# Kernel tuning notes

Measured on AMD Instinct MI355X. Metric: run time of the kernel, lower is better.

Reference implementation:

```python
import jax, jax.numpy as jnp
import numpy as np

N_VERTS = 1_000_000
N_EDGES = 3_000_000
H, W = 1024, 1024
MAX_DEPTH = 10.0
DEPTH_SCALE = 1.0
CREGU = 2000.0


def setup_inputs() -> dict:
    key = jax.random.key(0)
    k1, k2, k3, k4, k5, k6 = jax.random.split(key, 6)
    # mesh vertices roughly in a unit-radius blob
    vertices = jax.random.normal(k1, (N_VERTS, 3), dtype=jnp.float32) * 0.5
    vertices_ref = vertices + 0.01 * jax.random.normal(k2, (N_VERTS, 3), dtype=jnp.float32)
    quaternion = jax.random.normal(k3, (4,), dtype=jnp.float32) + jnp.array([0., 0., 0., 1.], jnp.float32)
    translation = jax.random.normal(k4, (3,), dtype=jnp.float32) * 0.05
    hand_image = jax.random.uniform(k5, (H, W), dtype=jnp.float32) * MAX_DEPTH
    # camera per MeshDepthFitterEnergy.setImage: R = diag(1,-1,-1), focal = 2*W
    object_center = np.zeros(3, np.float32)
    object_radius = 0.5
    camera_center = object_center + np.array([-0.5, 0.0, 5.0], np.float32) * object_radius
    R = np.array([[1., 0., 0.], [0., -1., 0.], [0., 0., -1.]], np.float32)
    T = -R.T.dot(camera_center)
    focal = 2.0 * W
    intrinsic = jnp.array([[focal, 0., W / 2.], [0., focal, H / 2.], [0., 0., 1.]], jnp.float32)
    extrinsic = jnp.array(np.column_stack((R, T)), jnp.float32)
    edges = jax.random.randint(k6, (N_EDGES, 2), 0, N_VERTS, dtype=jnp.int64)
    return {"vertices": vertices, "vertices_ref": vertices_ref, "quaternion": quaternion,
            "translation": translation, "hand_image": hand_image,
            "intrinsic": intrinsic, "extrinsic": extrinsic, "edges": edges}


def _qrot(q, v):
    # q: [4] (x,y,z,w) normalized; v: [N,3]
    qvec = q[:3]
    uv = jnp.cross(jnp.broadcast_to(qvec, v.shape), v)
    uuv = jnp.cross(jnp.broadcast_to(qvec, v.shape), uv)
    return v + 2.0 * (q[3] * uv + uuv)


def _forward(vertices, vertices_ref, quaternion, translation, hand_image,
             intrinsic, extrinsic, edges):
    # rigid transform
    q = quaternion / jnp.linalg.norm(quaternion)
    v_centered = vertices - jnp.mean(vertices, axis=0, keepdims=True)
    v_t = _qrot(q, v_centered) + translation  # [N,3]
    # camera projection: P_cam = R x + T ; pix = K P_cam / z
    p_cam = v_t @ extrinsic[:, :3].T + extrinsic[:, 3]  # [N,3]
    proj = p_cam @ intrinsic.T
    z = p_cam[:, 2] * DEPTH_SCALE
    u = proj[:, 0] / proj[:, 2]
    v = proj[:, 1] / proj[:, 2]
    xi = jnp.clip(jnp.round(u), 0, W - 1).astype(jnp.int32)
    yi = jnp.clip(jnp.round(v), 0, H - 1).astype(jnp.int32)
    flat = yi * W + xi  # [N]
    # z-buffer: scatter-min of per-vertex depth (invalid/behind-camera -> MAX_DEPTH)
    zvalid = jnp.where(z > 0, z, MAX_DEPTH)
    depth_flat = jnp.full((H * W,), MAX_DEPTH, dtype=vertices.dtype).at[flat].min(zvalid)
    depth = jnp.clip(depth_flat, 0.0, MAX_DEPTH).reshape(H, W)
    diff_image = (depth - hand_image) ** 2
    e_data = jnp.sum(diff_image)
    # Laplacian rigid energy: cregu * || L (V - Vref) ||^2 over the edge graph
    dv = vertices - vertices_ref
    src, dst = edges[:, 0], edges[:, 1]
    deg = jax.ops.segment_sum(jnp.ones((N_EDGES,), vertices.dtype), src, num_segments=N_VERTS)
    neigh = jax.ops.segment_sum(dv[dst], src, num_segments=N_VERTS)  # [N,3]
    ldv = deg[:, None] * dv - neigh
    e_rigid = CREGU * jnp.sum(ldv ** 2)
    return e_data + e_rigid


def reference(vertices, vertices_ref, quaternion, translation, hand_image,
              intrinsic, extrinsic, edges):
    return _forward(vertices, vertices_ref, quaternion, translation, hand_image,
                    intrinsic, extrinsic, edges)
```

## Files before the change

kernel.cpp:

```cpp
#include <hip/hip_runtime.h>

#define W_IMG 1024
#define H_IMG 1024
#define HW_IMG (W_IMG * H_IMG)
#define NV 1000000
#define NE 3000000
#define NV4 (NE / 2)
#define MAX_DEPTH 10.0f
#define CREGU 2000.0f

#define NBUCKET 245
#define BSHIFT 12
#define BSIZE 4096

#define PREP_BLOCKS 2048
#define HIST_BLOCKS 250
#define HIST_V4 6000
#define SCAT_V4 2048
#define SCAT_EDGES (SCAT_V4 * 2)
#define SCAT_BLOCKS ((NV4 + SCAT_V4 - 1) / SCAT_V4)
#define GEO_BLOCKS 1024
#define TSIZE 2048
#define EDATA_BLOCKS 256

#define QXY 4096.0f
#define IQXY 2.44140625e-4f
#define QZ 2048.0f
#define IQZ 4.8828125e-4f
#define BXY2 1024
#define BZ2 512

typedef int v4i __attribute__((ext_vector_type(4)));

__device__ __forceinline__ unsigned pack_dv32(float x, float y, float z) {
    x = fminf(fmaxf(x, -0.2f), 0.2f);
    y = fminf(fmaxf(y, -0.2f), 0.2f);
    z = fminf(fmaxf(z, -0.2f), 0.2f);
    unsigned px = (unsigned)((int)rintf(x * QXY) + BXY2);
    unsigned py = (unsigned)((int)rintf(y * QXY) + BXY2);
    unsigned pz = (unsigned)((int)rintf(z * QZ) + BZ2);
    return (px << 21) | (py << 10) | pz;
}

__device__ __forceinline__ unsigned long long expand_dv(unsigned p) {
    unsigned long long x = (p >> 21) & 0x7FFu;
    unsigned long long y = (p >> 10) & 0x7FFu;
    unsigned long long z = p & 0x3FFu;
    return (x << 44) | (y << 24) | (z << 6) | 1ull;
}

__device__ __forceinline__ float block_sum_256(float v, float* smem) {
#pragma unroll
    for (int o = 32; o > 0; o >>= 1) v += __shfl_down(v, o, 64);
    int lane = threadIdx.x & 63;
    int wid  = threadIdx.x >> 6;
    if (lane == 0) smem[wid] = v;
    __syncthreads();
    float r = 0.f;
    if (threadIdx.x == 0) r = smem[0] + smem[1] + smem[2] + smem[3];
    __syncthreads();
    return r;
}

__device__ __forceinline__ void prefix245(const unsigned* __restrict__ src,
                                          unsigned* dst) {
    int t = threadIdx.x;
    unsigned h = (t < NBUCKET) ? src[t] : 0u;
    dst[t] = h;
    __syncthreads();
#pragma unroll
    for (int o = 1; o < 256; o <<= 1) {
        unsigned v = (t >= o) ? dst[t - o] : 0u;
        __syncthreads();
        dst[t] += v;
        __syncthreads();
    }
    unsigned excl = dst[t] - h;
    __syncthreads();
    dst[t] = excl;
    __syncthreads();
}

__global__ void k_prep(const float* __restrict__ verts,
                       const float* __restrict__ verts_ref,
                       unsigned* __restrict__ pdv32,
                       unsigned* __restrict__ depth_bits, int ncd,
                       unsigned long long* __restrict__ neigh, int modeA,
                       const v4i* __restrict__ edges2,
                       unsigned* __restrict__ hist,
                       float4* __restrict__ partial) {
    __shared__ float smem[4];
    __shared__ unsigned lh[NBUCKET];
    int i = blockIdx.x * blockDim.x + threadIdx.x;
    int stride = gridDim.x * blockDim.x;

    float sx = 0.f, sy = 0.f, sz = 0.f;
    for (int j = i; j < NV; j += stride) {
        float x = verts[3 * j + 0];
        float y = verts[3 * j + 1];
        float z = verts[3 * j + 2];
        sx += x; sy += y; sz += z;
        pdv32[j] = pack_dv32(x - verts_ref[3 * j + 0],
                             y - verts_ref[3 * j + 1],
                             z - verts_ref[3 * j + 2]);
        if (!modeA) neigh[j] = 0ull;
    }
    size_t totd = (size_t)ncd * HW_IMG;
    for (size_t j = i; j < totd; j += stride) depth_bits[j] = 0x41200000u;

    if (modeA && blockIdx.x < HIST_BLOCKS) {
        for (int t = threadIdx.x; t < NBUCKET; t += blockDim.x) lh[t] = 0u;
        __syncthreads();
        int base = blockIdx.x * HIST_V4;
        for (int k = threadIdx.x; k < HIST_V4; k += blockDim.x) {
            v4i e = __builtin_nontemporal_load(&edges2[base + k]);
            atomicAdd(&lh[(unsigned)e.x >> BSHIFT], 1u);
            atomicAdd(&lh[(unsigned)e.z >> BSHIFT], 1u);
        }
        __syncthreads();
        for (int t = threadIdx.x; t < NBUCKET; t += blockDim.x)
            if (lh[t]) atomicAdd(&hist[t], lh[t]);
    }

    float bx = block_sum_256(sx, smem);
    float by = block_sum_256(sy, smem);
    float bz = block_sum_256(sz, smem);
    if (threadIdx.x == 0) {
        float4 p; p.x = bx; p.y = by; p.z = bz; p.w = 0.f;
        partial[blockIdx.x] = p;
    }
}

union SMem {
    struct {
        unsigned h_key[TSIZE];
        unsigned h_val[TSIZE];
        float rsm[8];
    } geo;
    struct {
        unsigned long long sort[SCAT_EDGES];
        unsigned sLh[NBUCKET];
        unsigned sPfx[256];
        unsigned sDelta[NBUCKET];
        unsigned sOff[256];
    } sc;
};

__global__ void k_main(const v4i* __restrict__ edges2,
                       const unsigned* __restrict__ pdv32,
                       unsigned long long* __restrict__ rec,
                       const unsigned* __restrict__ hist,
                       unsigned* __restrict__ reserve,
                       unsigned long long* __restrict__ neigh, int modeA,
                       const float* __restrict__ verts,
                       const float* __restrict__ quat,
                       const float* __restrict__ trans,
                       const float* __restrict__ intr,
                       const float* __restrict__ extr,
                       const float4* __restrict__ partial,
                       unsigned* __restrict__ depth_bits, int ncd) {
    __shared__ SMem sm;

    if (blockIdx.x >= GEO_BLOCKS) {
        int sb = blockIdx.x - GEO_BLOCKS;
        int base = sb * SCAT_V4;
        if (modeA) {
            for (int t = threadIdx.x; t < NBUCKET; t += blockDim.x) sm.sc.sLh[t] = 0u;
            __syncthreads();

            v4i e[8];
            unsigned r0[8], r1[8];
#pragma unroll
            for (int k = 0; k < 8; ++k) {
                int idx = base + k * 256 + (int)threadIdx.x;
                if (idx < NV4) {
                    e[k] = __builtin_nontemporal_load(&edges2[idx]);
                    r0[k] = atomicAdd(&sm.sc.sLh[(unsigned)e[k].x >> BSHIFT], 1u);
                    r1[k] = atomicAdd(&sm.sc.sLh[(unsigned)e[k].z >> BSHIFT], 1u);
                }
            }
            __syncthreads();
            prefix245(sm.sc.sLh, sm.sc.sPfx);
            prefix245(hist, sm.sc.sOff);
            for (int t = threadIdx.x; t < NBUCKET; t += blockDim.x) {
                unsigned c = sm.sc.sLh[t];
                unsigned res = c ? atomicAdd(&reserve[t], c) : 0u;
                sm.sc.sDelta[t] = sm.sc.sOff[t] + res - sm.sc.sPfx[t];
            }
            __syncthreads();
#pragma unroll
            for (int k = 0; k < 8; ++k) {
                int idx = base + k * 256 + (int)threadIdx.x;
                if (idx < NV4) {
                    unsigned s0 = (unsigned)e[k].x;
                    unsigned b0 = s0 >> BSHIFT;
                    unsigned long long rec0 =
                        ((unsigned long long)b0 << 56) |
                        ((unsigned long long)pdv32[e[k].y] << 12) |
                        (s0 & (BSIZE - 1));
                    sm.sc.sort[sm.sc.sPfx[b0] + r0[k]] = rec0;
                    unsigned s1 = (unsigned)e[k].z;
                    unsigned b1 = s1 >> BSHIFT;
                    unsigned long long rec1 =
                        ((unsigned long long)b1 << 56) |
                        ((unsigned long long)pdv32[e[k].w] << 12) |
                        (s1 & (BSIZE - 1));
                    sm.sc.sort[sm.sc.sPfx[b1] + r1[k]] = rec1;
                }
            }
            __syncthreads();
            int nrec = (base + SCAT_V4 <= NV4) ? SCAT_EDGES
                                               : 2 * (NV4 - base);
#pragma unroll
            for (int k = 0; k < 16; ++k) {
                int t = k * 256 + (int)threadIdx.x;
                if (t < nrec) {
                    unsigned long long r = sm.sc.sort[t];
                    unsigned bin = (unsigned)(r >> 56);
                    rec[(size_t)t + sm.sc.sDelta[bin]] = r;
                }
            }
        } else {
#pragma unroll
            for (int k = 0; k < 8; ++k) {
                int idx = base + k * 256 + (int)threadIdx.x;
                if (idx < NV4) {
                    v4i e = __builtin_nontemporal_load(&edges2[idx]);
                    atomicAdd(&neigh[(size_t)(unsigned)e.x], expand_dv(pdv32[e.y]));
                    atomicAdd(&neigh[(size_t)(unsigned)e.z], expand_dv(pdv32[e.w]));
                }
            }
        }
        return;
    }

    int gb = blockIdx.x;
    for (int s = threadIdx.x; s < TSIZE; s += blockDim.x) {
        sm.geo.h_key[s] = 0xFFFFFFFFu;
        sm.geo.h_val[s] = 0xFFFFFFFFu;
    }
    __syncthreads();

    float sx = 0.f, sy = 0.f, sz = 0.f;
    for (int p = threadIdx.x; p < PREP_BLOCKS; p += blockDim.x) {
        float4 v = partial[p];
        sx += v.x; sy += v.y; sz += v.z;
    }
    float bx = block_sum_256(sx, sm.geo.rsm);
    float by = block_sum_256(sy, sm.geo.rsm);
    float bz = block_sum_256(sz, sm.geo.rsm);
    if (threadIdx.x == 0) {
        const float inv_nv = 1.0f / (float)NV;
        sm.geo.rsm[4] = bx * inv_nv;
        sm.geo.rsm[5] = by * inv_nv;
        sm.geo.rsm[6] = bz * inv_nv;
    }
    __syncthreads();
    float mx = sm.geo.rsm[4], my = sm.geo.rsm[5], mz = sm.geo.rsm[6];

    float qx = quat[0], qy = quat[1], qz = quat[2], qw = quat[3];
    float qn = rsqrtf(qx * qx + qy * qy + qz * qz + qw * qw);
    qx *= qn; qy *= qn; qz *= qn; qw *= qn;
    float t0 = trans[0], t1 = trans[1], t2 = trans[2];
    float e0 = extr[0], e1 = extr[1], e2 = extr[2],  e3 = extr[3];
    float e4 = extr[4], e5 = extr[5], e6 = extr[6],  e7 = extr[7];
    float e8 = extr[8], e9 = extr[9], e10 = extr[10], e11 = extr[11];
    float i0 = intr[0], i1 = intr[1], i2 = intr[2];
    float i3 = intr[3], i4 = intr[4], i5 = intr[5];
    float i6 = intr[6], i7 = intr[7], i8 = intr[8];

    unsigned* __restrict__ db = depth_bits + (size_t)(gb & (ncd - 1)) * HW_IMG;

    int stride = GEO_BLOCKS * blockDim.x;
    for (int j = gb * blockDim.x + threadIdx.x; j < NV; j += stride) {
        float vx = __builtin_nontemporal_load(&verts[3 * j + 0]) - mx;
        float vy = __builtin_nontemporal_load(&verts[3 * j + 1]) - my;
        float vz = __builtin_nontemporal_load(&verts[3 * j + 2]) - mz;

        float uvx = qy * vz - qz * vy;
        float uvy = qz * vx - qx * vz;
        float uvz = qx * vy - qy * vx;
        float uuvx = qy * uvz - qz * uvy;
        float uuvy = qz * uvx - qx * uvz;
        float uuvz = qx * uvy - qy * uvx;
        float tx = vx + 2.f * (qw * uvx + uuvx) + t0;
        float ty = vy + 2.f * (qw * uvy + uuvy) + t1;
        float tz = vz + 2.f * (qw * uvz + uuvz) + t2;

        float px = e0 * tx + e1 * ty + e2  * tz + e3;
        float py = e4 * tx + e5 * ty + e6  * tz + e7;
        float pz = e8 * tx + e9 * ty + e10 * tz + e11;

        float pr0 = i0 * px + i1 * py + i2 * pz;
        float pr1 = i3 * px + i4 * py + i5 * pz;
        float pr2 = i6 * px + i7 * py + i8 * pz;

        float u = pr0 / pr2;
        float v = pr1 / pr2;
        float ru = rintf(u);
        float rv = rintf(v);
        bool border = (ru < 0.f) | (ru > (float)(W_IMG - 1)) |
                      (rv < 0.f) | (rv > (float)(H_IMG - 1));
        float xf = fminf(fmaxf(ru, 0.f), (float)(W_IMG - 1));
        float yf = fminf(fmaxf(rv, 0.f), (float)(H_IMG - 1));
        unsigned flat = (unsigned)((int)yf * W_IMG + (int)xf);

        if (pz > 0.f) {
            unsigned zbits = __float_as_uint(pz);
            bool direct = !border;
            if (border) {
                unsigned slot = (flat * 2654435761u) >> 21;
                bool done = false;
#pragma unroll
                for (int p = 0; p < 4; ++p) {
                    unsigned old = atomicCAS(&sm.geo.h_key[slot], 0xFFFFFFFFu, flat);
                    if (old == 0xFFFFFFFFu || old == flat) {
                        atomicMin(&sm.geo.h_val[slot], zbits);
                        done = true;
                        break;
                    }
                    slot = (slot + 1) & (TSIZE - 1);
                }
                direct = !done;
            }
            if (direct) atomicMin(&db[flat], zbits);
        }
    }
    __syncthreads();
    for (int s = threadIdx.x; s < TSIZE; s += blockDim.x) {
        unsigned k = sm.geo.h_key[s];
        if (k != 0xFFFFFFFFu) atomicMin(&db[k], sm.geo.h_val[s]);
    }
}

__global__ void k_energy(const unsigned* __restrict__ depth_bits, int ncd,
                         const float* __restrict__ hand,
                         const unsigned* __restrict__ pdv32,
                         const unsigned long long* __restrict__ rec,
                         const unsigned* __restrict__ hist,
                         const unsigned long long* __restrict__ neigh, int modeA,
                         float* out) {
    __shared__ unsigned long long acc[BSIZE];
    __shared__ unsigned sOff[256];
    __shared__ float smem[4];

    if (blockIdx.x < NBUCKET) {
        int b = blockIdx.x;
        int vbase = b * BSIZE;
        int nvert = (NV - vbase < BSIZE) ? (NV - vbase) : BSIZE;
        if (modeA) {
            prefix245(hist, sOff);
            unsigned start = sOff[b];
            unsigned count = hist[b];
            for (int v = threadIdx.x; v < BSIZE; v += blockDim.x) acc[v] = 0ull;
            __syncthreads();
            for (unsigned i = threadIdx.x; i < count; i += blockDim.x) {
                unsigned long long r = rec[start + i];
                unsigned p = (unsigned)(r >> 12);
                unsigned s = (unsigned)(r & (BSIZE - 1));
                atomicAdd(&acc[s], expand_dv(p));
            }
            __syncthreads();
        }
        float lacc = 0.f;
        for (int v = threadIdx.x; v < nvert; v += blockDim.x) {
            unsigned long long n = modeA ? acc[v] : neigh[(size_t)vbase + v];
            int cnt = (int)(n & 63ull);
            int rz  = (int)((n >> 6)  & 0x3FFFFull);
            int ry  = (int)((n >> 24) & 0xFFFFFull);
            int rx  = (int)(n >> 44);
            float nx = (float)(rx - cnt * BXY2) * IQXY;
            float ny = (float)(ry - cnt * BXY2) * IQXY;
            float nz = (float)(rz - cnt * BZ2)  * IQZ;
            unsigned p = pdv32[vbase + v];
            float dx = (float)((int)((p >> 21) & 0x7FFu) - BXY2) * IQXY;
            float dy = (float)((int)((p >> 10) & 0x7FFu) - BXY2) * IQXY;
            float dz = (float)((int)(p & 0x3FFu) - BZ2) * IQZ;
            float dg = (float)cnt;
            float lx = dg * dx - nx;
            float ly = dg * dy - ny;
            float lz = dg * dz - nz;
            lacc += lx * lx + ly * ly + lz * lz;
        }
        float bsum = block_sum_256(lacc, smem);
        if (threadIdx.x == 0) atomicAdd(out, CREGU * bsum);
    } else {
        int eb = blockIdx.x - NBUCKET;
        int i = eb * blockDim.x + threadIdx.x;
        int stride = EDATA_BLOCKS * blockDim.x;
        float accd = 0.f;
        for (int j = i; j < HW_IMG; j += stride) {
            float dmin = __uint_as_float(depth_bits[j]);
            for (int c = 1; c < ncd; ++c)
                dmin = fminf(dmin, __uint_as_float(depth_bits[(size_t)c * HW_IMG + j]));
            float depth = fminf(fmaxf(dmin, 0.f), MAX_DEPTH);
            float diff = depth - hand[j];
            accd += diff * diff;
        }
        float bsum = block_sum_256(accd, smem);
        if (threadIdx.x == 0) atomicAdd(out, bsum);
    }
}

extern "C" void kernel_launch(void* const* d_in, const int* in_sizes, int n_in,
                              void* d_out, int out_size, void* d_ws, size_t ws_size,
                              hipStream_t stream) {
    const float* verts     = (const float*)d_in[0];
    const float* verts_ref = (const float*)d_in[1];
    const float* quat      = (const float*)d_in[2];
    const float* trans     = (const float*)d_in[3];
    const float* hand      = (const float*)d_in[4];
    const float* intr      = (const float*)d_in[5];
    const float* extr      = (const float*)d_in[6];
    const int*   edges     = (const int*)d_in[7];
    float* out = (float*)d_out;

    char* ws = (char*)d_ws;
    const size_t OFF_BINS = (size_t)NV * 4;
    const size_t OFF_PART = OFF_BINS + 4096;
    const size_t OFF_REC  = OFF_PART + (size_t)PREP_BLOCKS * 16;

    const size_t A_FIX = OFF_REC + (size_t)NE * 8;
    const size_t B_FIX = OFF_REC + (size_t)NV * 8;

    int modeA, ncd;
    size_t OFF_DEPTH;
    if (ws_size >= A_FIX + 4ull * HW_IMG * 4)      { modeA = 1; ncd = 4; OFF_DEPTH = A_FIX; }
    else if (ws_size >= A_FIX + 2ull * HW_IMG * 4) { modeA = 1; ncd = 2; OFF_DEPTH = A_FIX; }
    else if (ws_size >= A_FIX + 1ull * HW_IMG * 4) { modeA = 1; ncd = 1; OFF_DEPTH = A_FIX; }
    else if (ws_size >= B_FIX + 4ull * HW_IMG * 4) { modeA = 0; ncd = 4; OFF_DEPTH = B_FIX; }
    else if (ws_size >= B_FIX + 2ull * HW_IMG * 4) { modeA = 0; ncd = 2; OFF_DEPTH = B_FIX; }
    else                                           { modeA = 0; ncd = 1; OFF_DEPTH = B_FIX; }

    unsigned*           pdv32      = (unsigned*)ws;
    unsigned*           hist       = (unsigned*)(ws + OFF_BINS);
    unsigned*           reserve    = hist + 256;
    float4*             partial    = (float4*)(ws + OFF_PART);
    unsigned long long* rec        = (unsigned long long*)(ws + OFF_REC);
    unsigned long long* neigh      = (unsigned long long*)(ws + OFF_REC);
    unsigned*           depth_bits = (unsigned*)(ws + OFF_DEPTH);

    const int B = 256;

    hipMemsetAsync(ws + OFF_BINS, 0, 4096, stream);
    hipMemsetAsync(d_out, 0, sizeof(float), stream);

    k_prep<<<PREP_BLOCKS, B, 0, stream>>>(verts, verts_ref, pdv32, depth_bits,
                                          ncd, neigh, modeA, (const v4i*)edges,
                                          hist, partial);
    k_main<<<GEO_BLOCKS + SCAT_BLOCKS, B, 0, stream>>>(
        (const v4i*)edges, pdv32, rec, hist, reserve, neigh, modeA,
        verts, quat, trans, intr, extr, partial, depth_bits, ncd);
    k_energy<<<NBUCKET + EDATA_BLOCKS, B, 0, stream>>>(
        depth_bits, ncd, hand, pdv32, rec, hist, neigh, modeA, out);
}
```

Baseline: 234.4 us.

## Drop memsets and global histogram atomics, vectorize prep and depth loops

Zeroing of the output and the reserve counters moves into k_prep, which removes the two hipMemsetAsync calls. The global atomic histogram becomes per-block partial histograms; each scatter block reduces these partials and takes a prefix, and block 0 publishes the bucket offsets for k_energy. Vertex prep, depth-buffer init and the data-energy loop now use float4/uint4 accesses, and the atomic-neighbour fallback mode is removed. The trade-off is that every scatter block redundantly reads 250 histogram partials, and the old smaller-workspace fallback path is gone.

```diff
diff --git a/kernel.cpp b/kernel.cpp
--- a/kernel.cpp
+++ b/kernel.cpp
@@ -4,6 +4,7 @@
 #define H_IMG 1024
 #define HW_IMG (W_IMG * H_IMG)
 #define NV 1000000
+#define NQUAD (NV / 4)
 #define NE 3000000
 #define NV4 (NE / 2)
 #define MAX_DEPTH 10.0f
@@ -13,7 +14,7 @@
 #define BSHIFT 12
 #define BSIZE 4096
 
-#define PREP_BLOCKS 2048
+#define PREP_BLOCKS 1024
 #define HIST_BLOCKS 250
 #define HIST_V4 6000
 #define SCAT_V4 2048
@@ -62,54 +63,65 @@
     return r;
 }
 
-__device__ __forceinline__ void prefix245(const unsigned* __restrict__ src,
-                                          unsigned* dst) {
+__device__ __forceinline__ void prefix_excl_256(unsigned h, unsigned* buf) {
     int t = threadIdx.x;
-    unsigned h = (t < NBUCKET) ? src[t] : 0u;
-    dst[t] = h;
+    buf[t] = h;
     __syncthreads();
 #pragma unroll
     for (int o = 1; o < 256; o <<= 1) {
-        unsigned v = (t >= o) ? dst[t - o] : 0u;
-        __syncthreads();
-        dst[t] += v;
-        __syncthreads();
-    }
-    unsigned excl = dst[t] - h;
-    __syncthreads();
-    dst[t] = excl;
-    __syncthreads();
-}
-
-__global__ void k_prep(const float* __restrict__ verts,
-                       const float* __restrict__ verts_ref,
-                       unsigned* __restrict__ pdv32,
-                       unsigned* __restrict__ depth_bits, int ncd,
-                       unsigned long long* __restrict__ neigh, int modeA,
+        unsigned v = (t >= o) ? buf[t - o] : 0u;
+        __syncthreads();
+        buf[t] += v;
+        __syncthreads();
+    }
+    unsigned excl = buf[t] - h;
+    __syncthreads();
+    buf[t] = excl;
+    __syncthreads();
+}
+
+__global__ void k_prep(const float4* __restrict__ verts4,
+                       const float4* __restrict__ ref4,
+                       uint4* __restrict__ pdv4,
+                       uint4* __restrict__ depth4, int ncd,
                        const v4i* __restrict__ edges2,
-                       unsigned* __restrict__ hist,
-                       float4* __restrict__ partial) {
+                       unsigned* __restrict__ hist_part,
+                       unsigned* __restrict__ reserve,
+                       float4* __restrict__ partial, float* out) {
     __shared__ float smem[4];
-    __shared__ unsigned lh[NBUCKET];
+    __shared__ unsigned lh[256];
     int i = blockIdx.x * blockDim.x + threadIdx.x;
     int stride = gridDim.x * blockDim.x;
 
     float sx = 0.f, sy = 0.f, sz = 0.f;
-    for (int j = i; j < NV; j += stride) {
-        float x = verts[3 * j + 0];
-        float y = verts[3 * j + 1];
-        float z = verts[3 * j + 2];
-        sx += x; sy += y; sz += z;
-        pdv32[j] = pack_dv32(x - verts_ref[3 * j + 0],
-                             y - verts_ref[3 * j + 1],
-                             z - verts_ref[3 * j + 2]);
-        if (!modeA) neigh[j] = 0ull;
-    }
-    size_t totd = (size_t)ncd * HW_IMG;
-    for (size_t j = i; j < totd; j += stride) depth_bits[j] = 0x41200000u;
-
-    if (modeA && blockIdx.x < HIST_BLOCKS) {
-        for (int t = threadIdx.x; t < NBUCKET; t += blockDim.x) lh[t] = 0u;
+    for (int t = i; t < NQUAD; t += stride) {
+        float4 a = verts4[3 * t + 0];
+        float4 b = verts4[3 * t + 1];
+        float4 c = verts4[3 * t + 2];
+        float4 ra = ref4[3 * t + 0];
+        float4 rb = ref4[3 * t + 1];
+        float4 rc = ref4[3 * t + 2];
+        sx += a.x + a.w + b.z + c.y;
+        sy += a.y + b.x + b.w + c.z;
+        sz += a.z + b.y + c.x + c.w;
+        uint4 q;
+        q.x = pack_dv32(a.x - ra.x, a.y - ra.y, a.z - ra.z);
+        q.y = pack_dv32(a.w - ra.w, b.x - rb.x, b.y - rb.y);
+        q.z = pack_dv32(b.z - rb.z, b.w - rb.w, c.x - rc.x);
+        q.w = pack_dv32(c.y - rc.y, c.z - rc.z, c.w - rc.w);
+        pdv4[t] = q;
+    }
+    int tot4 = ncd * (HW_IMG / 4);
+    uint4 dinit = make_uint4(0x41200000u, 0x41200000u, 0x41200000u, 0x41200000u);
+    for (int j = i; j < tot4; j += stride) depth4[j] = dinit;
+
+    if (blockIdx.x == 0) {
+        reserve[threadIdx.x] = 0u;
+        if (threadIdx.x == 0) out[0] = 0.f;
+    }
+
+    if (blockIdx.x < HIST_BLOCKS) {
+        lh[threadIdx.x] = 0u;
         __syncthreads();
         int base = blockIdx.x * HIST_V4;
         for (int k = threadIdx.x; k < HIST_V4; k += blockDim.x) {
@@ -118,8 +130,7 @@
             atomicAdd(&lh[(unsigned)e.z >> BSHIFT], 1u);
         }
         __syncthreads();
-        for (int t = threadIdx.x; t < NBUCKET; t += blockDim.x)
-            if (lh[t]) atomicAdd(&hist[t], lh[t]);
+        hist_part[blockIdx.x * 256 + threadIdx.x] = lh[threadIdx.x];
     }
 
     float bx = block_sum_256(sx, smem);
@@ -139,9 +150,9 @@
     } geo;
     struct {
         unsigned long long sort[SCAT_EDGES];
-        unsigned sLh[NBUCKET];
+        unsigned sLh[256];
         unsigned sPfx[256];
-        unsigned sDelta[NBUCKET];
+        unsigned sDelta[256];
         unsigned sOff[256];
     } sc;
 };
@@ -149,9 +160,9 @@
 __global__ void k_main(const v4i* __restrict__ edges2,
                        const unsigned* __restrict__ pdv32,
                        unsigned long long* __restrict__ rec,
-                       const unsigned* __restrict__ hist,
+                       const unsigned* __restrict__ hist_part,
+                       unsigned* __restrict__ gpfx,
                        unsigned* __restrict__ reserve,
-                       unsigned long long* __restrict__ neigh, int modeA,
                        const float* __restrict__ verts,
                        const float* __restrict__ quat,
                        const float* __restrict__ trans,
@@ -163,72 +174,62 @@
 
     if (blockIdx.x >= GEO_BLOCKS) {
         int sb = blockIdx.x - GEO_BLOCKS;
+        int tid = threadIdx.x;
+        unsigned tot = 0u;
+        if (tid < NBUCKET)
+            for (int b = 0; b < HIST_BLOCKS; ++b) tot += hist_part[b * 256 + tid];
+        prefix_excl_256((tid < NBUCKET) ? tot : 0u, sm.sc.sOff);
+        if (sb == 0) gpfx[tid] = sm.sc.sOff[tid];
+
         int base = sb * SCAT_V4;
-        if (modeA) {
-            for (int t = threadIdx.x; t < NBUCKET; t += blockDim.x) sm.sc.sLh[t] = 0u;
-            __syncthreads();
-
-            v4i e[8];
-            unsigned r0[8], r1[8];
-#pragma unroll
-            for (int k = 0; k < 8; ++k) {
-                int idx = base + k * 256 + (int)threadIdx.x;
-                if (idx < NV4) {
-                    e[k] = __builtin_nontemporal_load(&edges2[idx]);
-                    r0[k] = atomicAdd(&sm.sc.sLh[(unsigned)e[k].x >> BSHIFT], 1u);
-                    r1[k] = atomicAdd(&sm.sc.sLh[(unsigned)e[k].z >> BSHIFT], 1u);
-                }
+        sm.sc.sLh[tid] = 0u;
+        __syncthreads();
+        v4i e[8];
+        unsigned r0[8], r1[8];
+#pragma unroll
+        for (int k = 0; k < 8; ++k) {
+            int idx = base + k * 256 + tid;
+            if (idx < NV4) {
+                e[k] = __builtin_nontemporal_load(&edges2[idx]);
+                r0[k] = atomicAdd(&sm.sc.sLh[(unsigned)e[k].x >> BSHIFT], 1u);
+                r1[k] = atomicAdd(&sm.sc.sLh[(unsigned)e[k].z >> BSHIFT], 1u);
             }
-            __syncthreads();
-            prefix245(sm.sc.sLh, sm.sc.sPfx);
-            prefix245(hist, sm.sc.sOff);
-            for (int t = threadIdx.x; t < NBUCKET; t += blockDim.x) {
-                unsigned c = sm.sc.sLh[t];
-                unsigned res = c ? atomicAdd(&reserve[t], c) : 0u;
-                sm.sc.sDelta[t] = sm.sc.sOff[t] + res - sm.sc.sPfx[t];
+        }
+        __syncthreads();
+        unsigned cnt = sm.sc.sLh[tid];
+        prefix_excl_256((tid < NBUCKET) ? cnt : 0u, sm.sc.sPfx);
+        if (tid < NBUCKET) {
+            unsigned res = cnt ? atomicAdd(&reserve[tid], cnt) : 0u;
+            sm.sc.sDelta[tid] = sm.sc.sOff[tid] + res - sm.sc.sPfx[tid];
+        }
+        __syncthreads();
+#pragma unroll
+        for (int k = 0; k < 8; ++k) {
+            int idx = base + k * 256 + tid;
+            if (idx < NV4) {
+                unsigned s0 = (unsigned)e[k].x;
+                unsigned b0 = s0 >> BSHIFT;
+                sm.sc.sort[sm.sc.sPfx[b0] + r0[k]] =
+                    ((unsigned long long)b0 << 56) |
+                    ((unsigned long long)pdv32[e[k].y] << 12) |
+                    (s0 & (BSIZE - 1));
+                unsigned s1 = (unsigned)e[k].z;
+                unsigned b1 = s1 >> BSHIFT;
+                sm.sc.sort[sm.sc.sPfx[b1] + r1[k]] =
+                    ((unsigned long long)b1 << 56) |
+                    ((unsigned long long)pdv32[e[k].w] << 12) |
+                    (s1 & (BSIZE - 1));
             }
-            __syncthreads();
-#pragma unroll
-            for (int k = 0; k < 8; ++k) {
-                int idx = base + k * 256 + (int)threadIdx.x;
-                if (idx < NV4) {
-                    unsigned s0 = (unsigned)e[k].x;
-                    unsigned b0 = s0 >> BSHIFT;
-                    unsigned long long rec0 =
-                        ((unsigned long long)b0 << 56) |
-                        ((unsigned long long)pdv32[e[k].y] << 12) |
-                        (s0 & (BSIZE - 1));
-                    sm.sc.sort[sm.sc.sPfx[b0] + r0[k]] = rec0;
-                    unsigned s1 = (unsigned)e[k].z;
-                    unsigned b1 = s1 >> BSHIFT;
-                    unsigned long long rec1 =
-                        ((unsigned long long)b1 << 56) |
-                        ((unsigned long long)pdv32[e[k].w] << 12) |
-                        (s1 & (BSIZE - 1));
-                    sm.sc.sort[sm.sc.sPfx[b1] + r1[k]] = rec1;
-                }
-            }
-            __syncthreads();
-            int nrec = (base + SCAT_V4 <= NV4) ? SCAT_EDGES
-                                               : 2 * (NV4 - base);
-#pragma unroll
-            for (int k = 0; k < 16; ++k) {
-                int t = k * 256 + (int)threadIdx.x;
-                if (t < nrec) {
-                    unsigned long long r = sm.sc.sort[t];
-                    unsigned bin = (unsigned)(r >> 56);
-                    rec[(size_t)t + sm.sc.sDelta[bin]] = r;
-                }
-            }
-        } else {
-#pragma unroll
-            for (int k = 0; k < 8; ++k) {
-                int idx = base + k * 256 + (int)threadIdx.x;
-                if (idx < NV4) {
-                    v4i e = __builtin_nontemporal_load(&edges2[idx]);
-                    atomicAdd(&neigh[(size_t)(unsigned)e.x], expand_dv(pdv32[e.y]));
-                    atomicAdd(&neigh[(size_t)(unsigned)e.z], expand_dv(pdv32[e.w]));
-                }
+        }
+        __syncthreads();
+        int nrec = (base + SCAT_V4 <= NV4) ? SCAT_EDGES : 2 * (NV4 - base);
+#pragma unroll
+        for (int k = 0; k < 16; ++k) {
+            int t = k * 256 + tid;
+            if (t < nrec) {
+                unsigned long long r = sm.sc.sort[t];
+                unsigned bin = (unsigned)(r >> 56);
+                rec[(size_t)t + sm.sc.sDelta[bin]] = r;
             }
         }
         return;
@@ -334,37 +335,31 @@
 }
 
 __global__ void k_energy(const unsigned* __restrict__ depth_bits, int ncd,
-                         const float* __restrict__ hand,
+                         const float4* __restrict__ hand4,
                          const unsigned* __restrict__ pdv32,
                          const unsigned long long* __restrict__ rec,
-                         const unsigned* __restrict__ hist,
-                         const unsigned long long* __restrict__ neigh, int modeA,
+                         const unsigned* __restrict__ gpfx,
                          float* out) {
     __shared__ unsigned long long acc[BSIZE];
-    __shared__ unsigned sOff[256];
     __shared__ float smem[4];
 
     if (blockIdx.x < NBUCKET) {
         int b = blockIdx.x;
         int vbase = b * BSIZE;
         int nvert = (NV - vbase < BSIZE) ? (NV - vbase) : BSIZE;
-        if (modeA) {
-            prefix245(hist, sOff);
-            unsigned start = sOff[b];
-            unsigned count = hist[b];
-            for (int v = threadIdx.x; v < BSIZE; v += blockDim.x) acc[v] = 0ull;
-            __syncthreads();
-            for (unsigned i = threadIdx.x; i < count; i += blockDim.x) {
-                unsigned long long r = rec[start + i];
-                unsigned p = (unsigned)(r >> 12);
-                unsigned s = (unsigned)(r & (BSIZE - 1));
-                atomicAdd(&acc[s], expand_dv(p));
-            }
-            __syncthreads();
-        }
+        unsigned start = gpfx[b];
+        unsigned count = gpfx[b + 1] - start;
+        for (int v = threadIdx.x; v < BSIZE; v += blockDim.x) acc[v] = 0ull;
+        __syncthreads();
+        for (unsigned i = threadIdx.x; i < count; i += blockDim.x) {
+            unsigned long long r = rec[start + i];
+            atomicAdd(&acc[(unsigned)(r & (BSIZE - 1))],
+                      expand_dv((unsigned)(r >> 12)));
+        }
+        __syncthreads();
         float lacc = 0.f;
         for (int v = threadIdx.x; v < nvert; v += blockDim.x) {
-            unsigned long long n = modeA ? acc[v] : neigh[(size_t)vbase + v];
+            unsigned long long n = acc[v];
             int cnt = (int)(n & 63ull);
             int rz  = (int)((n >> 6)  & 0x3FFFFull);
             int ry  = (int)((n >> 24) & 0xFFFFFull);
@@ -386,16 +381,27 @@
         if (threadIdx.x == 0) atomicAdd(out, CREGU * bsum);
     } else {
         int eb = blockIdx.x - NBUCKET;
+        const uint4* d4 = (const uint4*)depth_bits;
         int i = eb * blockDim.x + threadIdx.x;
         int stride = EDATA_BLOCKS * blockDim.x;
         float accd = 0.f;
-        for (int j = i; j < HW_IMG; j += stride) {
-            float dmin = __uint_as_float(depth_bits[j]);
-            for (int c = 1; c < ncd; ++c)
-                dmin = fminf(dmin, __uint_as_float(depth_bits[(size_t)c * HW_IMG + j]));
-            float depth = fminf(fmaxf(dmin, 0.f), MAX_DEPTH);
-            float diff = depth - hand[j];
-            accd += diff * diff;
+        for (int j = i; j < HW_IMG / 4; j += stride) {
+            uint4 d = d4[j];
+            float m0 = __uint_as_float(d.x), m1 = __uint_as_float(d.y);
+            float m2 = __uint_as_float(d.z), m3 = __uint_as_float(d.w);
+            for (int c = 1; c < ncd; ++c) {
+                uint4 dc = d4[(size_t)c * (HW_IMG / 4) + j];
+                m0 = fminf(m0, __uint_as_float(dc.x));
+                m1 = fminf(m1, __uint_as_float(dc.y));
+                m2 = fminf(m2, __uint_as_float(dc.z));
+                m3 = fminf(m3, __uint_as_float(dc.w));
+            }
+            float4 h = hand4[j];
+            float f0 = fminf(fmaxf(m0, 0.f), MAX_DEPTH) - h.x;
+            float f1 = fminf(fmaxf(m1, 0.f), MAX_DEPTH) - h.y;
+            float f2 = fminf(fmaxf(m2, 0.f), MAX_DEPTH) - h.z;
+            float f3 = fminf(fmaxf(m3, 0.f), MAX_DEPTH) - h.w;
+            accd += f0 * f0 + f1 * f1 + f2 * f2 + f3 * f3;
         }
         float bsum = block_sum_256(accd, smem);
         if (threadIdx.x == 0) atomicAdd(out, bsum);
@@ -416,41 +422,33 @@
     float* out = (float*)d_out;
 
     char* ws = (char*)d_ws;
-    const size_t OFF_BINS = (size_t)NV * 4;
-    const size_t OFF_PART = OFF_BINS + 4096;
-    const size_t OFF_REC  = OFF_PART + (size_t)PREP_BLOCKS * 16;
-
-    const size_t A_FIX = OFF_REC + (size_t)NE * 8;
-    const size_t B_FIX = OFF_REC + (size_t)NV * 8;
-
-    int modeA, ncd;
-    size_t OFF_DEPTH;
-    if (ws_size >= A_FIX + 4ull * HW_IMG * 4)      { modeA = 1; ncd = 4; OFF_DEPTH = A_FIX; }
-    else if (ws_size >= A_FIX + 2ull * HW_IMG * 4) { modeA = 1; ncd = 2; OFF_DEPTH = A_FIX; }
-    else if (ws_size >= A_FIX + 1ull * HW_IMG * 4) { modeA = 1; ncd = 1; OFF_DEPTH = A_FIX; }
-    else if (ws_size >= B_FIX + 4ull * HW_IMG * 4) { modeA = 0; ncd = 4; OFF_DEPTH = B_FIX; }
-    else if (ws_size >= B_FIX + 2ull * HW_IMG * 4) { modeA = 0; ncd = 2; OFF_DEPTH = B_FIX; }
-    else                                           { modeA = 0; ncd = 1; OFF_DEPTH = B_FIX; }
+    const size_t OFF_GPFX = (size_t)NV * 4;
+    const size_t OFF_PART = OFF_GPFX + 1024;
+    const size_t OFF_HP   = OFF_PART + (size_t)PREP_BLOCKS * 16;
+    const size_t OFF_RSV  = OFF_HP + (size_t)HIST_BLOCKS * 256 * 4;
+    const size_t OFF_REC  = OFF_RSV + 1024;
+    const size_t OFF_DEP  = OFF_REC + (size_t)NE * 8;
+
+    int ncd = (ws_size >= OFF_DEP + 4ull * HW_IMG * 4) ? 4
+            : (ws_size >= OFF_DEP + 2ull * HW_IMG * 4) ? 2 : 1;
 
     unsigned*           pdv32      = (unsigned*)ws;
-    unsigned*           hist       = (unsigned*)(ws + OFF_BINS);
-    unsigned*           reserve    = hist + 256;
+    unsigned*           gpfx       = (unsigned*)(ws + OFF_GPFX);
     float4*             partial    = (float4*)(ws + OFF_PART);
+    unsigned*           hist_part  = (unsigned*)(ws + OFF_HP);
+    unsigned*           reserve    = (unsigned*)(ws + OFF_RSV);
     unsigned long long* rec        = (unsigned long long*)(ws + OFF_REC);
-    unsigned long long* neigh      = (unsigned long long*)(ws + OFF_REC);
-    unsigned*           depth_bits = (unsigned*)(ws + OFF_DEPTH);
+    unsigned*           depth_bits = (unsigned*)(ws + OFF_DEP);
 
     const int B = 256;
 
-    hipMemsetAsync(ws + OFF_BINS, 0, 4096, stream);
-    hipMemsetAsync(d_out, 0, sizeof(float), stream);
-
-    k_prep<<<PREP_BLOCKS, B, 0, stream>>>(verts, verts_ref, pdv32, depth_bits,
-                                          ncd, neigh, modeA, (const v4i*)edges,
-                                          hist, partial);
+    k_prep<<<PREP_BLOCKS, B, 0, stream>>>(
+        (const float4*)verts, (const float4*)verts_ref, (uint4*)pdv32,
+        (uint4*)depth_bits, ncd, (const v4i*)edges, hist_part, reserve,
+        partial, out);
     k_main<<<GEO_BLOCKS + SCAT_BLOCKS, B, 0, stream>>>(
-        (const v4i*)edges, pdv32, rec, hist, reserve, neigh, modeA,
+        (const v4i*)edges, pdv32, rec, hist_part, gpfx, reserve,
         verts, quat, trans, intr, extr, partial, depth_bits, ncd);
     k_energy<<<NBUCKET + EDATA_BLOCKS, B, 0, stream>>>(
-        depth_bits, ncd, hand, pdv32, rec, hist, neigh, modeA, out);
-}
+        depth_bits, ncd, (const float4*)hand, pdv32, rec, gpfx, out);
+}
```

After: 235.9 us (median of 2 runs). About the same (+0.7%).
